# Kernel tuning notes

Hardware: AMD Instinct MI355X
Metric: run time of the kernel (lower is better)

The kernel has to match this reference:

```python
import jax, jax.numpy as jnp
import numpy as np

P_F, P_E = 64, 64
S_F, S_E = 64, 64
W_F, W_E = 32, 32
FH, FO = 256, 128
PR_F, PR_E = 32, 32
VI_F, VI_E = 32, 32
RE_F, RE_E = 32, 32
H1, H2 = 64, 32
GH, NHEADS = 32, 4
DH = PR_E + VI_E + RE_E + P_E + S_E  # 224, hypernetwork input dim
FUSE_IN = 2 * P_E + 2 * S_E + W_E    # 288
N_COLL = 200000
M_NODES = 2048


def setup_inputs() -> dict:
    key = jax.random.key(0)
    ks = jax.random.split(key, 40)
    rn = lambda k, s, sc=1.0: jax.random.normal(k, s, jnp.float32) * sc
    W = 0.05
    inp = {
        'x_u_profile': rn(ks[0], (1, P_F)),
        'x_u_shopping': rn(ks[1], (1, S_F)),
        'x_u_workplace': rn(ks[2], (1, W_F)),
        'x_u_colleague_p': rn(ks[3], (N_COLL, P_F)),
        'x_u_colleague_s': rn(ks[4], (N_COLL, S_F)),
        'x_h_property': rn(ks[5], (1, PR_F)),
        'x_h_vicinity': rn(ks[6], (1, VI_F)),
        'x_h_reachability': rn(ks[7], (1, RE_F)),
        'x_h_neighborhood_p': rn(ks[8], (M_NODES, P_F)),
        'x_h_neighborhood_s': rn(ks[9], (M_NODES, S_F)),
        'x_h_neighborhood_g': jax.random.randint(ks[10], (M_NODES, M_NODES), 0, 2, jnp.int32),
        'W_up': rn(ks[11], (P_F, P_E), W), 'b_up': jnp.zeros((P_E,), jnp.float32),
        'W_us': rn(ks[12], (S_F, S_E), W), 'b_us': jnp.zeros((S_E,), jnp.float32),
        'W_uw': rn(ks[13], (W_F, W_E), W), 'b_uw': jnp.zeros((W_E,), jnp.float32),
        'v_w': rn(ks[14], (2 * (P_E + S_E), 1), W),
        'W_f1': rn(ks[15], (FUSE_IN, FH), W), 'b_f1': jnp.zeros((FH,), jnp.float32),
        'W_f2': rn(ks[16], (FH, FO), W), 'b_f2': jnp.zeros((FO,), jnp.float32),
        'W_m1': rn(ks[17], (FO, DH * H1), W), 'b_m1': jnp.zeros((DH * H1,), jnp.float32),
        'W_m2': rn(ks[18], (FO, H1 * H2), W), 'b_m2': jnp.zeros((H1 * H2,), jnp.float32),
        'W_m3': rn(ks[19], (FO, H2), W), 'b_m3': jnp.zeros((H2,), jnp.float32),
        'W_hp': rn(ks[20], (PR_F, PR_E), W), 'b_hp': jnp.zeros((PR_E,), jnp.float32),
        'W_hv': rn(ks[21], (VI_F, VI_E), W), 'b_hv': jnp.zeros((VI_E,), jnp.float32),
        'W_hr': rn(ks[22], (RE_F, RE_E), W), 'b_hr': jnp.zeros((RE_E,), jnp.float32),
        'Wg': rn(ks[23], (NHEADS, P_E + S_E, GH), W),
        'ag': rn(ks[24], (NHEADS, 2 * GH, 1), W),
        'Wo': rn(ks[25], (NHEADS * GH, P_E + S_E), W),
        'ao': rn(ks[26], (2 * (P_E + S_E), 1), W),
    }
    return inp


def _forward(x_u_profile, x_u_shopping, x_u_workplace, x_u_colleague_p, x_u_colleague_s,
             x_h_property, x_h_vicinity, x_h_reachability,
             x_h_neighborhood_p, x_h_neighborhood_s,
             W_up, b_up, W_us, b_us, W_uw, b_uw, v_w,
             W_f1, b_f1, W_f2, b_f2,
             W_m1, b_m1, W_m2, b_m2, W_m3, b_m3,
             W_hp, b_hp, W_hv, b_hv, W_hr, b_hr,
             Wg, ag, Wo, ao, adj):
    celu, relu = jax.nn.celu, jax.nn.relu
    # user embeddings (batch = 1)
    u_p = celu(x_u_profile @ W_up + b_up)    # [1, P_E]
    u_s = celu(x_u_shopping @ W_us + b_us)   # [1, S_E]
    u_w = celu(x_u_workplace @ W_uw + b_uw)  # [1, W_E]
    # colleague embeddings (shared embedding weights)
    c_p = celu(x_u_colleague_p @ W_up + b_up)  # [N, P_E]
    c_s = celu(x_u_colleague_s @ W_us + b_us)  # [N, S_E]
    n = c_p.shape[0]
    # expand user (shopping, profile) to colleague set and attend
    exp = jnp.concatenate([jnp.broadcast_to(u_s, (n, S_E)),
                           jnp.broadcast_to(u_p, (n, P_E))], axis=1)
    concat = jnp.concatenate([exp, c_p, c_s], axis=1)        # [N, 2*(P_E+S_E)]
    atten = jax.nn.softmax(concat @ v_w, axis=0)             # [N, 1]
    coll = jnp.concatenate([c_p, c_s], axis=1)               # [N, P_E+S_E]
    x_coll = (atten.T @ coll) / n                            # [1, P_E+S_E]
    # user fusion
    fu = jnp.concatenate([u_p, u_s, u_w, x_coll], axis=1)    # [1, FUSE_IN]
    x_u = celu(celu(fu @ W_f1 + b_f1) @ W_f2 + b_f2)         # [1, FO]
    # hypernetwork-generated weights
    w1 = celu(x_u @ W_m1 + b_m1).reshape(DH, H1)
    w2 = celu(x_u @ W_m2 + b_m2).reshape(H1, H2)
    w3 = celu(x_u @ W_m3 + b_m3).reshape(H2, 1)
    # house embeddings
    h_p = celu(x_h_property @ W_hp + b_hp)
    h_v = celu(x_h_vicinity @ W_hv + b_hv)
    h_r = celu(x_h_reachability @ W_hr + b_hr)
    # neighborhood GAT over dense adjacency
    n_p = celu(x_h_neighborhood_p @ W_up + b_up)
    n_s = celu(x_h_neighborhood_s @ W_us + b_us)
    gx = jnp.concatenate([n_p, n_s], axis=1)                 # [M, P_E+S_E]
    mask = adj > 0

    def gat_layer(x, Wl, al):
        h = x @ Wl                                            # [M, F]
        f = h.shape[1]
        f1 = h @ al[:f]                                       # [M, 1]
        f2 = h @ al[f:]                                       # [M, 1]
        e = jax.nn.leaky_relu(f1 + f2.T, 0.2)                 # [M, M]
        e = jnp.where(mask, e, -1e9)
        att = jax.nn.softmax(e, axis=1)
        return att @ h

    heads = jax.vmap(lambda Wl, al: jax.nn.elu(gat_layer(gx, Wl, al)))(Wg, ag)  # [H, M, GH]
    hcat = jnp.transpose(heads, (1, 0, 2)).reshape(gx.shape[0], NHEADS * GH)
    gat_out = jax.nn.elu(gat_layer(hcat, Wo, ao))             # [M, P_E+S_E]
    neigh = gat_out.mean(axis=0, keepdims=True)               # [1, P_E+S_E]
    x_h = jnp.concatenate([h_p, h_v, h_r, neigh], axis=1)     # [1, DH]
    # meta_fcn: per-user generated MLP applied to house features
    return jax.nn.sigmoid(relu(relu(x_h @ w1) @ w2) @ w3)     # [1, 1]


def reference(x_u_profile, x_u_shopping, x_u_workplace, x_u_colleague_p, x_u_colleague_s,
              x_h_property, x_h_vicinity, x_h_reachability,
              x_h_neighborhood_p, x_h_neighborhood_s, x_h_neighborhood_g,
              W_up, b_up, W_us, b_us, W_uw, b_uw, v_w,
              W_f1, b_f1, W_f2, b_f2,
              W_m1, b_m1, W_m2, b_m2, W_m3, b_m3,
              W_hp, b_hp, W_hv, b_hv, W_hr, b_hr,
              Wg, ag, Wo, ao):
    return _forward(x_u_profile, x_u_shopping, x_u_workplace, x_u_colleague_p, x_u_colleague_s,
                    x_h_property, x_h_vicinity, x_h_reachability,
                    x_h_neighborhood_p, x_h_neighborhood_s,
                    W_up, b_up, W_us, b_us, W_uw, b_uw, v_w,
                    W_f1, b_f1, W_f2, b_f2,
                    W_m1, b_m1, W_m2, b_m2, W_m3, b_m3,
                    W_hp, b_hp, W_hv, b_hv, W_hr, b_hr,
                    Wg, ag, Wo, ao, x_h_neighborhood_g)
```

## Files before the change

kernel.cpp:

```cpp
#include <hip/hip_runtime.h>
#include <math.h>

#define N_COLL 200000

typedef const float* fp;
typedef __attribute__((ext_vector_type(8))) short bf16x8;
typedef __attribute__((ext_vector_type(4))) float f32x4;

#define WS_UP    0
#define WS_US    64
#define WS_UW    128
#define WS_HP    160
#define WS_HV    192
#define WS_HR    224
#define WS_XU    384
#define WS_W1    512
#define WS_W2    14848
#define WS_W3    16896
#define WS_NEIGH 16928
#define WS_CSUM  18976
#define WS_GX    23552
#define WS_HT1   285696
#define WS_F1G   416768
#define WS_F2G   424960
#define WS_HCAT  433152
#define WS_HT2   695296
#define WS_F1O   826368
#define WS_F2O   828416
#define WS_MASK  830464

__device__ __forceinline__ float celu1(float x){
    return fmaxf(x, 0.f) + __expf(fminf(x, 0.f)) - 1.f;
}
__device__ __forceinline__ float rl(float x, int k){
    return __int_as_float(__builtin_amdgcn_readlane(__float_as_int(x), k));
}
__device__ __forceinline__ short f2bf(float f){
    return (short)(__float_as_uint(f) >> 16);
}
__device__ __forceinline__ bf16x8 pack8(f32x4 a, f32x4 b){
    bf16x8 r;
    r[0]=f2bf(a[0]); r[1]=f2bf(a[1]); r[2]=f2bf(a[2]); r[3]=f2bf(a[3]);
    r[4]=f2bf(b[0]); r[5]=f2bf(b[1]); r[6]=f2bf(b[2]); r[7]=f2bf(b[3]);
    return r;
}

__global__ __launch_bounds__(256) void kA(
    fp Xcp, fp Xcs, fp vw,
    fp xup, fp xus, fp xuw, fp xhp, fp xhv, fp xhr,
    fp Wup, fp bup, fp Wus, fp bus, fp Wuw, fp buw,
    fp Whp, fp bhp, fp Whv, fp bhv, fp Whr, fp bhr,
    fp Xnp, fp Xns, const int* __restrict__ adj, float* ws)
{
    __shared__ float smem[8720];
    int t = threadIdx.x;
    int b = blockIdx.x;
    if (b < 768){
        float* sW = smem;
        float* sRed = smem + 8192;
        for (int i = t; i < 4096; i += 256){ sW[i] = Wup[i]; sW[4096+i] = Wus[i]; }
        __syncthreads();
        const int lane = t & 63, wv = t >> 6;
        const int q = lane >> 4, c16 = lane & 15;

        bf16x8 B[2][2][4];
        float bias[8], vv[8];
        #pragma unroll
        for (int mat = 0; mat < 2; ++mat)
          #pragma unroll
          for (int ks = 0; ks < 2; ++ks)
            #pragma unroll
            for (int ct = 0; ct < 4; ++ct){
                bf16x8 f;
                #pragma unroll
                for (int j = 0; j < 8; ++j)
                    f[j] = f2bf(sW[mat*4096 + (ks*32 + q*8 + j)*64 + ct*16 + c16]);
                B[mat][ks][ct] = f;
            }
        #pragma unroll
        for (int tt = 0; tt < 8; ++tt){
            int gcol = tt*16 + c16;
            bias[tt] = (tt < 4) ? bup[gcol] : bus[gcol-64];
            vv[tt]   = vw[128 + gcol];
        }

        const int wave = b*4 + wv;
        float accw[8] = {0,0,0,0,0,0,0,0};
        float accl = 0.f;

        int rt = wave;
        f32x4 L[8];
        {
            int row = rt*16 + c16;
            const float* xp = Xcp + row*64 + q*8;
            const float* xs = Xcs + row*64 + q*8;
            L[0]=*(const f32x4*)(xp);    L[1]=*(const f32x4*)(xp+4);
            L[2]=*(const f32x4*)(xp+32); L[3]=*(const f32x4*)(xp+36);
            L[4]=*(const f32x4*)(xs);    L[5]=*(const f32x4*)(xs+4);
            L[6]=*(const f32x4*)(xs+32); L[7]=*(const f32x4*)(xs+36);
        }
        while (rt < 12500){
            int nrt = rt + 3072;
            f32x4 N[8];
            if (nrt < 12500){
                int row = nrt*16 + c16;
                const float* xp = Xcp + row*64 + q*8;
                const float* xs = Xcs + row*64 + q*8;
                N[0]=*(const f32x4*)(xp);    N[1]=*(const f32x4*)(xp+4);
                N[2]=*(const f32x4*)(xp+32); N[3]=*(const f32x4*)(xp+36);
                N[4]=*(const f32x4*)(xs);    N[5]=*(const f32x4*)(xs+4);
                N[6]=*(const f32x4*)(xs+32); N[7]=*(const f32x4*)(xs+36);
            }
            bf16x8 Ap0 = pack8(L[0],L[1]);
            bf16x8 Ap1 = pack8(L[2],L[3]);
            bf16x8 As0 = pack8(L[4],L[5]);
            bf16x8 As1 = pack8(L[6],L[7]);

            float cel[8][4];
            float logit[4] = {0,0,0,0};
            #pragma unroll
            for (int tt = 0; tt < 8; ++tt){
                int ct = tt & 3;
                f32x4 c = {0.f,0.f,0.f,0.f};
                if (tt < 4){
                    c = __builtin_amdgcn_mfma_f32_16x16x32_bf16(Ap0, B[0][0][ct], c, 0,0,0);
                    c = __builtin_amdgcn_mfma_f32_16x16x32_bf16(Ap1, B[0][1][ct], c, 0,0,0);
                } else {
                    c = __builtin_amdgcn_mfma_f32_16x16x32_bf16(As0, B[1][0][ct], c, 0,0,0);
                    c = __builtin_amdgcn_mfma_f32_16x16x32_bf16(As1, B[1][1][ct], c, 0,0,0);
                }
                #pragma unroll
                for (int r = 0; r < 4; ++r){
                    float v = celu1(c[r] + bias[tt]);
                    cel[tt][r] = v;
                    logit[r] = fmaf(v, vv[tt], logit[r]);
                }
            }
            #pragma unroll
            for (int d = 1; d < 16; d <<= 1){
                #pragma unroll
                for (int r = 0; r < 4; ++r) logit[r] += __shfl_xor(logit[r], d);
            }
            float p[4];
            #pragma unroll
            for (int r = 0; r < 4; ++r){ p[r] = __expf(logit[r]); accl += p[r]; }
            #pragma unroll
            for (int tt = 0; tt < 8; ++tt)
                #pragma unroll
                for (int r = 0; r < 4; ++r) accw[tt] = fmaf(p[r], cel[tt][r], accw[tt]);
            #pragma unroll
            for (int i = 0; i < 8; ++i) L[i] = N[i];
            rt = nrt;
        }
        #pragma unroll
        for (int tt = 0; tt < 8; ++tt){
            accw[tt] += __shfl_xor(accw[tt], 16);
            accw[tt] += __shfl_xor(accw[tt], 32);
        }
        accl += __shfl_xor(accl, 16);
        accl += __shfl_xor(accl, 32);
        if (q == 0){
            #pragma unroll
            for (int tt = 0; tt < 8; ++tt) sRed[wv*132 + tt*16 + c16] = accw[tt];
        }
        if (lane == 0) sRed[wv*132 + 128] = accl;
        __syncthreads();
        if (t < 129){
            float s = sRed[t] + sRed[132+t] + sRed[264+t] + sRed[396+t];
            atomicAdd(ws + WS_CSUM + (b & 31)*132 + t, s);
        }
    } else if (b < 1280){
        unsigned* mb = (unsigned*)(ws + WS_MASK);
        int idx = (b-768)*256 + t;
        const int* a = adj + (idx>>6)*2048 + (idx&63)*32;
        unsigned bits = 0u;
        #pragma unroll 8
        for (int j = 0; j < 32; ++j) bits |= (a[j] > 0 ? 1u : 0u) << j;
        mb[idx] = bits;
    } else if (b < 1408){
        float* sWp = smem;
        float* sWs = smem + 4096;
        float* sbp = smem + 8192;
        float* sbs = smem + 8256;
        int b2 = b - 1280;
        for (int i = t; i < 4096; i += 256){ sWp[i] = Wup[i]; sWs[i] = Wus[i]; }
        if (t < 64){ sbp[t]=bup[t]; sbs[t]=bus[t]; }
        __syncthreads();
        int lane = t & 63, wave = (b2<<2) | (t>>6);
        for (int r = wave; r < 2048; r += 512){
            float xp = Xnp[(r<<6)+lane], xs = Xns[(r<<6)+lane];
            float cp = sbp[lane], cs = sbs[lane];
            #pragma unroll 8
            for (int k = 0; k < 64; ++k){
                cp = fmaf(rl(xp,k), sWp[(k<<6)+lane], cp);
                cs = fmaf(rl(xs,k), sWs[(k<<6)+lane], cs);
            }
            ws[WS_GX + (r<<7) + lane]      = celu1(cp);
            ws[WS_GX + (r<<7) + 64 + lane] = celu1(cs);
        }
    } else {
        if (t < 64){
            float acc = bup[t];
            for (int k = 0; k < 64; ++k) acc = fmaf(xup[k], Wup[k*64+t], acc);
            ws[WS_UP+t] = celu1(acc);
        } else if (t < 128){
            int j = t-64; float acc = bus[j];
            for (int k = 0; k < 64; ++k) acc = fmaf(xus[k], Wus[k*64+j], acc);
            ws[WS_US+j] = celu1(acc);
        } else if (t < 160){
            int j = t-128; float acc = buw[j];
            for (int k = 0; k < 32; ++k) acc = fmaf(xuw[k], Wuw[k*32+j], acc);
            ws[WS_UW+j] = celu1(acc);
        } else if (t < 192){
            int j = t-160; float acc = bhp[j];
            for (int k = 0; k < 32; ++k) acc = fmaf(xhp[k], Whp[k*32+j], acc);
            ws[WS_HP+j] = celu1(acc);
        } else if (t < 224){
            int j = t-192; float acc = bhv[j];
            for (int k = 0; k < 32; ++k) acc = fmaf(xhv[k], Whv[k*32+j], acc);
            ws[WS_HV+j] = celu1(acc);
        } else {
            int j = t-224; float acc = bhr[j];
            for (int k = 0; k < 32; ++k) acc = fmaf(xhr[k], Whr[k*32+j], acc);
            ws[WS_HR+j] = celu1(acc);
        }
    }
}

__global__ __launch_bounds__(256) void kB(fp Wg, fp ag, fp Wf1, fp bf1, fp Wf2, fp bf2, float* ws){
    __shared__ float smem[673];
    int t = threadIdx.x;
    int b = blockIdx.x;
    if (b < 128){
        int lane = t & 63;
        int wave = (b<<2) | (t>>6);
        int h1 = lane>>5, h2 = 2 + (lane>>5), g = lane & 31;
        float agh1a = ag[h1*64+g], agh1b = ag[h1*64+32+g];
        float agh2a = ag[h2*64+g], agh2b = ag[h2*64+32+g];
        unsigned short* ht = (unsigned short*)(ws + WS_HT1);
        for (int r = wave; r < 2048; r += 512){
            const float* gx = ws + WS_GX + (r<<7);
            float x1 = gx[lane], x2 = gx[64+lane];
            float a1 = 0.f, a2 = 0.f;
            #pragma unroll 4
            for (int k = 0; k < 64; ++k){
                float gk = rl(x1,k);
                a1 = fmaf(gk, Wg[h1*4096 + (k<<5) + g], a1);
                a2 = fmaf(gk, Wg[h2*4096 + (k<<5) + g], a2);
            }
            #pragma unroll 4
            for (int k = 0; k < 64; ++k){
                float gk = rl(x2,k);
                a1 = fmaf(gk, Wg[h1*4096 + ((64+k)<<5) + g], a1);
                a2 = fmaf(gk, Wg[h2*4096 + ((64+k)<<5) + g], a2);
            }
            ht[lane*2048 + r]      = (unsigned short)f2bf(a1);
            ht[(64+lane)*2048 + r] = (unsigned short)f2bf(a2);
            float s1 = a1*agh1a, t1 = a1*agh1b, s2 = a2*agh2a, t2 = a2*agh2b;
            #pragma unroll
            for (int d = 1; d < 32; d <<= 1){
                s1 += __shfl_xor(s1,d); t1 += __shfl_xor(t1,d);
                s2 += __shfl_xor(s2,d); t2 += __shfl_xor(t2,d);
            }
            if ((lane&31) == 0){
                int hh = lane>>5;
                ws[WS_F1G + (hh<<11) + r] = s1;
                ws[WS_F2G + (hh<<11) + r] = t1;
                ws[WS_F1G + ((hh+2)<<11) + r] = s2;
                ws[WS_F2G + ((hh+2)<<11) + r] = t2;
            }
        }
    } else {
        float* fu  = smem;
        float* hid = smem + 288;
        float* cs  = smem + 544;
        if (t < 129){
            float s = 0.f;
            #pragma unroll
            for (int k = 0; k < 32; ++k) s += ws[WS_CSUM + k*132 + t];
            cs[t] = s;
        }
        if (t < 64)       fu[t] = ws[WS_UP + t];
        else if (t < 128) fu[t] = ws[WS_US + t-64];
        else if (t < 160) fu[t] = ws[WS_UW + t-128];
        __syncthreads();
        if (t < 128) fu[160 + t] = cs[t] / (cs[128] * (float)N_COLL);
        __syncthreads();
        float acc = bf1[t];
        for (int k = 0; k < 288; ++k) acc = fmaf(fu[k], Wf1[k*256+t], acc);
        hid[t] = celu1(acc);
        __syncthreads();
        if (t < 128){
            float a2 = bf2[t];
            for (int k = 0; k < 256; ++k) a2 = fmaf(hid[k], Wf2[k*128+t], a2);
            ws[WS_XU + t] = celu1(a2);
        }
    }
}

__global__ __launch_bounds__(256) void kC(fp Wm1, fp bm1, fp Wm2, fp bm2, fp Wm3, fp bm3, float* ws){
    __shared__ float smem[2112];
    int t = threadIdx.x;
    int b = blockIdx.x;
    if (b < 512){
        float* Cs = smem;
        float* Sp = smem + 2048;
        int w = t >> 6, lane = t & 63;
        int q = lane >> 4, c16 = lane & 15;
        int rt = b >> 2, h = b & 3;
        int row = rt*16 + c16;
        const unsigned* mb = (const unsigned*)(ws + WS_MASK) + row*64;
        const unsigned short* HT = (const unsigned short*)(ws + WS_HT1) + h*32*2048;
        float f1 = ws[WS_F1G + (h<<11) + row];
        const float* f2 = ws + WS_F2G + (h<<11);
        f32x4 c0 = {0,0,0,0}, c1 = {0,0,0,0};
        float S = 0.f;
        for (int kt = w*16; kt < w*16 + 16; ++kt){
            unsigned m32 = mb[kt];
            const float* f2p = f2 + kt*32 + q*8;
            f32x4 fa = *(const f32x4*)(f2p);
            f32x4 fb = *(const f32x4*)(f2p+4);
            bf16x8 A;
            #pragma unroll
            for (int j = 0; j < 8; ++j){
                float e = f1 + ((j<4) ? fa[j] : fb[j-4]);
                e = fmaxf(e, 0.2f*e);
                float p = ((m32 >> (q*8+j)) & 1u) ? __expf(e) : 0.f;
                unsigned short pb = (unsigned short)(__float_as_uint(p) >> 16);
                A[j] = (short)pb;
                S += __uint_as_float(((unsigned)pb) << 16);
            }
            bf16x8 B0 = *(const bf16x8*)(HT + (c16)*2048    + kt*32 + q*8);
            bf16x8 B1 = *(const bf16x8*)(HT + (16+c16)*2048 + kt*32 + q*8);
            c0 = __builtin_amdgcn_mfma_f32_16x16x32_bf16(A, B0, c0, 0,0,0);
            c1 = __builtin_amdgcn_mfma_f32_16x16x32_bf16(A, B1, c1, 0,0,0);
        }
        S += __shfl_xor(S, 16);
        S += __shfl_xor(S, 32);
        if (q == 0) Sp[w*16 + c16] = S;
        #pragma unroll
        for (int r = 0; r < 4; ++r){
            Cs[w*512 + (q*4+r)*32 + c16]      = c0[r];
            Cs[w*512 + (q*4+r)*32 + 16 + c16] = c1[r];
        }
        __syncthreads();
        for (int ee = t; ee < 512; ee += 256){
            int r = ee >> 5, cc = ee & 31;
            float v = Cs[r*32+cc] + Cs[512 + r*32+cc] + Cs[1024 + r*32+cc] + Cs[1536 + r*32+cc];
            float Ss = Sp[r] + Sp[16+r] + Sp[32+r] + Sp[48+r];
            ws[WS_HCAT + (rt*16 + r)*128 + h*32 + cc] = celu1(v / Ss);
        }
    } else {
        float* xu = smem;
        if (t < 128) xu[t] = ws[WS_XU + t];
        __syncthreads();
        int j = (b - 512)*256 + t;
        if (j < 14336){
            float acc = bm1[j];
            for (int k = 0; k < 128; ++k) acc = fmaf(xu[k], Wm1[k*14336 + j], acc);
            ws[WS_W1 + j] = celu1(acc);
        } else if (j < 16384){
            int j2 = j - 14336;
            float acc = bm2[j2];
            for (int k = 0; k < 128; ++k) acc = fmaf(xu[k], Wm2[k*2048 + j2], acc);
            ws[WS_W2 + j2] = celu1(acc);
        } else if (j < 16416){
            int j3 = j - 16384;
            float acc = bm3[j3];
            for (int k = 0; k < 128; ++k) acc = fmaf(xu[k], Wm3[k*32 + j3], acc);
            ws[WS_W3 + j3] = celu1(acc);
        }
    }
}

__global__ __launch_bounds__(256) void l2_proj(fp Wo, fp ao, float* ws){
    int t = threadIdx.x, lane = t & 63;
    int wave = (blockIdx.x<<2) | (t>>6);
    float aoa1 = ao[lane],     aoa2 = ao[64+lane];
    float aob1 = ao[128+lane], aob2 = ao[192+lane];
    unsigned short* ht = (unsigned short*)(ws + WS_HT2);
    for (int r = wave; r < 2048; r += 512){
        const float* hc = ws + WS_HCAT + (r<<7);
        float x1 = hc[lane], x2 = hc[64+lane];
        float a1 = 0.f, a2 = 0.f;
        #pragma unroll 4
        for (int k = 0; k < 64; ++k){
            float gk = rl(x1,k);
            a1 = fmaf(gk, Wo[(k<<7)+lane], a1);
            a2 = fmaf(gk, Wo[(k<<7)+64+lane], a2);
        }
        #pragma unroll 4
        for (int k = 0; k < 64; ++k){
            float gk = rl(x2,k);
            a1 = fmaf(gk, Wo[((64+k)<<7)+lane], a1);
            a2 = fmaf(gk, Wo[((64+k)<<7)+64+lane], a2);
        }
        ht[lane*2048 + r]      = (unsigned short)f2bf(a1);
        ht[(64+lane)*2048 + r] = (unsigned short)f2bf(a2);
        float s = a1*aoa1 + a2*aoa2;
        float u = a1*aob1 + a2*aob2;
        #pragma unroll
        for (int d = 1; d < 64; d <<= 1){ s += __shfl_xor(s,d); u += __shfl_xor(u,d); }
        if (lane == 0){ ws[WS_F1O + r] = s; ws[WS_F2O + r] = u; }
    }
}

__global__ __launch_bounds__(256) void attend2(float* ws){
    __shared__ float Cs[4][16][128];
    __shared__ float Sp[4][16];
    __shared__ float colp[2][128];
    int t = threadIdx.x;
    int w = t >> 6, lane = t & 63;
    int q = lane >> 4, c16 = lane & 15;
    int rt = blockIdx.x;
    int row = rt*16 + c16;
    const unsigned* mb = (const unsigned*)(ws + WS_MASK) + row*64;
    const unsigned short* HT = (const unsigned short*)(ws + WS_HT2);
    float f1 = ws[WS_F1O + row];
    const float* f2 = ws + WS_F2O;
    f32x4 c[8];
    #pragma unroll
    for (int nt = 0; nt < 8; ++nt) c[nt] = (f32x4){0,0,0,0};
    float S = 0.f;
    for (int kt = w*16; kt < w*16 + 16; ++kt){
        unsigned m32 = mb[kt];
        const float* f2p = f2 + kt*32 + q*8;
        f32x4 fa = *(const f32x4*)(f2p);
        f32x4 fb = *(const f32x4*)(f2p+4);
        bf16x8 A;
        #pragma unroll
        for (int j = 0; j < 8; ++j){
            float e = f1 + ((j<4) ? fa[j] : fb[j-4]);
            e = fmaxf(e, 0.2f*e);
            float p = ((m32 >> (q*8+j)) & 1u) ? __expf(e) : 0.f;
            unsigned short pb = (unsigned short)(__float_as_uint(p) >> 16);
            A[j] = (short)pb;
            S += __uint_as_float(((unsigned)pb) << 16);
        }
        #pragma unroll
        for (int nt = 0; nt < 8; ++nt){
            bf16x8 B = *(const bf16x8*)(HT + (nt*16 + c16)*2048 + kt*32 + q*8);
            c[nt] = __builtin_amdgcn_mfma_f32_16x16x32_bf16(A, B, c[nt], 0,0,0);
        }
    }
    S += __shfl_xor(S, 16);
    S += __shfl_xor(S, 32);
    if (q == 0) Sp[w][c16] = S;
    #pragma unroll
    for (int nt = 0; nt < 8; ++nt)
        #pragma unroll
        for (int r = 0; r < 4; ++r)
            Cs[w][q*4+r][nt*16+c16] = c[nt][r];
    __syncthreads();
    int col = t & 127, half = t >> 7;
    float part = 0.f;
    for (int r = half*8; r < half*8 + 8; ++r){
        float v = Cs[0][r][col] + Cs[1][r][col] + Cs[2][r][col] + Cs[3][r][col];
        float Ss = Sp[0][r] + Sp[1][r] + Sp[2][r] + Sp[3][r];
        part += celu1(v / Ss);
    }
    colp[half][col] = part;
    __syncthreads();
    if (t < 128) atomicAdd(ws + WS_NEIGH + (blockIdx.x & 15)*128 + t, colp[0][t] + colp[1][t]);
}

__global__ __launch_bounds__(256) void final_k(float* ws, float* out){
    __shared__ float xh[224], r1[64], r2[32];
    int t = threadIdx.x;
    if (t < 32)       xh[t]      = ws[WS_HP + t];
    else if (t < 64)  xh[t]      = ws[WS_HV + t-32];
    else if (t < 96)  xh[t]      = ws[WS_HR + t-64];
    if (t < 128){
        float s = 0.f;
        #pragma unroll
        for (int k = 0; k < 16; ++k) s += ws[WS_NEIGH + k*128 + t];
        xh[96 + t] = s * (1.f/2048.f);
    }
    __syncthreads();
    if (t < 64){
        float acc = 0.f;
        for (int k = 0; k < 224; ++k) acc = fmaf(xh[k], ws[WS_W1 + k*64 + t], acc);
        r1[t] = fmaxf(acc, 0.f);
    }
    __syncthreads();
    if (t < 32){
        float acc = 0.f;
        for (int k = 0; k < 64; ++k) acc = fmaf(r1[k], ws[WS_W2 + k*32 + t], acc);
        r2[t] = fmaxf(acc, 0.f);
    }
    __syncthreads();
    if (t == 0){
        float acc = 0.f;
        for (int k = 0; k < 32; ++k) acc = fmaf(r2[k], ws[WS_W3 + k], acc);
        out[0] = 1.f / (1.f + __expf(-acc));
    }
}

extern "C" void kernel_launch(void* const* d_in, const int* in_sizes, int n_in,
                              void* d_out, int out_size, void* d_ws, size_t ws_size,
                              hipStream_t stream)
{
    fp xup = (fp)d_in[0],  xus = (fp)d_in[1],  xuw = (fp)d_in[2];
    fp Xcp = (fp)d_in[3],  Xcs = (fp)d_in[4];
    fp xhp = (fp)d_in[5],  xhv = (fp)d_in[6],  xhr = (fp)d_in[7];
    fp Xnp = (fp)d_in[8],  Xns = (fp)d_in[9];
    const int* adj = (const int*)d_in[10];
    fp Wup = (fp)d_in[11], bup = (fp)d_in[12];
    fp Wus = (fp)d_in[13], bus = (fp)d_in[14];
    fp Wuw = (fp)d_in[15], buw = (fp)d_in[16];
    fp vw  = (fp)d_in[17];
    fp Wf1 = (fp)d_in[18], bf1 = (fp)d_in[19];
    fp Wf2 = (fp)d_in[20], bf2 = (fp)d_in[21];
    fp Wm1 = (fp)d_in[22], bm1 = (fp)d_in[23];
    fp Wm2 = (fp)d_in[24], bm2 = (fp)d_in[25];
    fp Wm3 = (fp)d_in[26], bm3 = (fp)d_in[27];
    fp Whp = (fp)d_in[28], bhp = (fp)d_in[29];
    fp Whv = (fp)d_in[30], bhv = (fp)d_in[31];
    fp Whr = (fp)d_in[32], bhr = (fp)d_in[33];
    fp Wg  = (fp)d_in[34], ag  = (fp)d_in[35];
    fp Wo  = (fp)d_in[36], ao  = (fp)d_in[37];
    float* ws = (float*)d_ws;
    float* out = (float*)d_out;

    hipMemsetAsync((char*)d_ws + WS_NEIGH*sizeof(float), 0, 6272*sizeof(float), stream);

    kA<<<1409, 256, 0, stream>>>(Xcp,Xcs,vw, xup,xus,xuw,xhp,xhv,xhr,
                                 Wup,bup,Wus,bus,Wuw,buw,Whp,bhp,Whv,bhv,Whr,bhr,
                                 Xnp,Xns, adj, ws);
    kB<<<129, 256, 0, stream>>>(Wg, ag, Wf1,bf1,Wf2,bf2, ws);
    kC<<<577, 256, 0, stream>>>(Wm1,bm1,Wm2,bm2,Wm3,bm3, ws);
    l2_proj<<<128, 256, 0, stream>>>(Wo, ao, ws);
    attend2<<<128, 256, 0, stream>>>(ws);
    final_k<<<1, 256, 0, stream>>>(ws, out);
}
```

Before: 349.2 us.

## Fuse all stages into one persistent kernel with grid-wide barriers

Merges the six kernel launches into one 512-block persistent kernel that separates stages with software grid barriers built on atomic counters in workspace. The Wg and Wo projections are redone with bf16 MFMA tiles in place of scalar readlane FMA loops, the adjacency-mask and small-projection work is redistributed over fewer blocks, and the colleague-encoder loop now covers more rows per wave. This removes launch gaps and speeds the projections, at the cost of a spin barrier that deadlocks unless all 512 blocks are co-resident, and less parallelism in the colleague scan.

```diff
diff --git a/kernel.cpp b/kernel.cpp
--- a/kernel.cpp
+++ b/kernel.cpp
@@ -6,6 +6,7 @@
 typedef const float* fp;
 typedef __attribute__((ext_vector_type(8))) short bf16x8;
 typedef __attribute__((ext_vector_type(4))) float f32x4;
+typedef __attribute__((ext_vector_type(4))) short s16x4;
 
 #define WS_UP    0
 #define WS_US    64
@@ -19,6 +20,7 @@
 #define WS_W3    16896
 #define WS_NEIGH 16928
 #define WS_CSUM  18976
+#define WS_BAR   23200
 #define WS_GX    23552
 #define WS_HT1   285696
 #define WS_F1G   416768
@@ -45,49 +47,62 @@
     return r;
 }
 
-__global__ __launch_bounds__(256) void kA(
-    fp Xcp, fp Xcs, fp vw,
-    fp xup, fp xus, fp xuw, fp xhp, fp xhv, fp xhr,
-    fp Wup, fp bup, fp Wus, fp bus, fp Wuw, fp buw,
+#define GRID_N 512u
+__device__ __forceinline__ void gbar(float* ws, int which){
+    unsigned* c = (unsigned*)(ws + WS_BAR) + which;
+    __syncthreads();
+    if (threadIdx.x == 0){
+        __threadfence();
+        atomicAdd(c, 1u);
+        while (atomicAdd(c, 0u) < GRID_N) __builtin_amdgcn_s_sleep(8);
+        __threadfence();
+    }
+    __syncthreads();
+}
+
+__global__ __launch_bounds__(256, 2) void mega(
+    fp xup, fp xus, fp xuw, fp Xcp, fp Xcs,
+    fp xhp, fp xhv, fp xhr, fp Xnp, fp Xns, const int* __restrict__ adj,
+    fp Wup, fp bup, fp Wus, fp bus, fp Wuw, fp buw, fp vw,
+    fp Wf1, fp bf1, fp Wf2, fp bf2,
+    fp Wm1, fp bm1, fp Wm2, fp bm2, fp Wm3, fp bm3,
     fp Whp, fp bhp, fp Whv, fp bhv, fp Whr, fp bhr,
-    fp Xnp, fp Xns, const int* __restrict__ adj, float* ws)
+    fp Wg, fp ag, fp Wo, fp ao,
+    float* ws, float* out)
 {
-    __shared__ float smem[8720];
-    int t = threadIdx.x;
-    int b = blockIdx.x;
-    if (b < 768){
-        float* sW = smem;
-        float* sRed = smem + 8192;
-        for (int i = t; i < 4096; i += 256){ sW[i] = Wup[i]; sW[4096+i] = Wus[i]; }
-        __syncthreads();
-        const int lane = t & 63, wv = t >> 6;
-        const int q = lane >> 4, c16 = lane & 15;
-
+    __shared__ float smem[8512];
+    const int t = threadIdx.x;
+    const int b = blockIdx.x;
+    const int lane = t & 63, wv = t >> 6;
+    const int q = lane >> 4, c16 = lane & 15;
+
+    if (b < 384){
+        float* sRed = smem;
         bf16x8 B[2][2][4];
         float bias[8], vv[8];
         #pragma unroll
-        for (int mat = 0; mat < 2; ++mat)
-          #pragma unroll
-          for (int ks = 0; ks < 2; ++ks)
-            #pragma unroll
-            for (int ct = 0; ct < 4; ++ct){
-                bf16x8 f;
+        for (int mat = 0; mat < 2; ++mat){
+            fp W = mat ? Wus : Wup;
+            #pragma unroll
+            for (int ks = 0; ks < 2; ++ks)
                 #pragma unroll
-                for (int j = 0; j < 8; ++j)
-                    f[j] = f2bf(sW[mat*4096 + (ks*32 + q*8 + j)*64 + ct*16 + c16]);
-                B[mat][ks][ct] = f;
-            }
+                for (int ct = 0; ct < 4; ++ct){
+                    bf16x8 f;
+                    #pragma unroll
+                    for (int j = 0; j < 8; ++j)
+                        f[j] = f2bf(W[(ks*32 + q*8 + j)*64 + ct*16 + c16]);
+                    B[mat][ks][ct] = f;
+                }
+        }
         #pragma unroll
         for (int tt = 0; tt < 8; ++tt){
             int gcol = tt*16 + c16;
             bias[tt] = (tt < 4) ? bup[gcol] : bus[gcol-64];
             vv[tt]   = vw[128 + gcol];
         }
-
         const int wave = b*4 + wv;
         float accw[8] = {0,0,0,0,0,0,0,0};
         float accl = 0.f;
-
         int rt = wave;
         f32x4 L[8];
         {
@@ -100,7 +115,7 @@
             L[6]=*(const f32x4*)(xs+32); L[7]=*(const f32x4*)(xs+36);
         }
         while (rt < 12500){
-            int nrt = rt + 3072;
+            int nrt = rt + 1536;
             f32x4 N[8];
             if (nrt < 12500){
                 int row = nrt*16 + c16;
@@ -115,7 +130,6 @@
             bf16x8 Ap1 = pack8(L[2],L[3]);
             bf16x8 As0 = pack8(L[4],L[5]);
             bf16x8 As1 = pack8(L[6],L[7]);
-
             float cel[8][4];
             float logit[4] = {0,0,0,0};
             #pragma unroll
@@ -169,25 +183,54 @@
             float s = sRed[t] + sRed[132+t] + sRed[264+t] + sRed[396+t];
             atomicAdd(ws + WS_CSUM + (b & 31)*132 + t, s);
         }
-    } else if (b < 1280){
+    } else if (b < 448){
         unsigned* mb = (unsigned*)(ws + WS_MASK);
-        int idx = (b-768)*256 + t;
-        const int* a = adj + (idx>>6)*2048 + (idx&63)*32;
-        unsigned bits = 0u;
-        #pragma unroll 8
-        for (int j = 0; j < 32; ++j) bits |= (a[j] > 0 ? 1u : 0u) << j;
-        mb[idx] = bits;
-    } else if (b < 1408){
+        #pragma unroll
+        for (int s = 0; s < 8; ++s){
+            int idx = (b-384)*2048 + s*256 + t;
+            const int* a = adj + (idx>>6)*2048 + (idx&63)*32;
+            unsigned bits = 0u;
+            #pragma unroll 8
+            for (int j = 0; j < 32; ++j) bits |= (a[j] > 0 ? 1u : 0u) << j;
+            mb[idx] = bits;
+        }
+        if (b == 384){
+            if (t < 64){
+                float acc = bup[t];
+                for (int k = 0; k < 64; ++k) acc = fmaf(xup[k], Wup[k*64+t], acc);
+                ws[WS_UP+t] = celu1(acc);
+            } else if (t < 128){
+                int j = t-64; float acc = bus[j];
+                for (int k = 0; k < 64; ++k) acc = fmaf(xus[k], Wus[k*64+j], acc);
+                ws[WS_US+j] = celu1(acc);
+            } else if (t < 160){
+                int j = t-128; float acc = buw[j];
+                for (int k = 0; k < 32; ++k) acc = fmaf(xuw[k], Wuw[k*32+j], acc);
+                ws[WS_UW+j] = celu1(acc);
+            } else if (t < 192){
+                int j = t-160; float acc = bhp[j];
+                for (int k = 0; k < 32; ++k) acc = fmaf(xhp[k], Whp[k*32+j], acc);
+                ws[WS_HP+j] = celu1(acc);
+            } else if (t < 224){
+                int j = t-192; float acc = bhv[j];
+                for (int k = 0; k < 32; ++k) acc = fmaf(xhv[k], Whv[k*32+j], acc);
+                ws[WS_HV+j] = celu1(acc);
+            } else {
+                int j = t-224; float acc = bhr[j];
+                for (int k = 0; k < 32; ++k) acc = fmaf(xhr[k], Whr[k*32+j], acc);
+                ws[WS_HR+j] = celu1(acc);
+            }
+        }
+    } else {
         float* sWp = smem;
         float* sWs = smem + 4096;
         float* sbp = smem + 8192;
         float* sbs = smem + 8256;
-        int b2 = b - 1280;
         for (int i = t; i < 4096; i += 256){ sWp[i] = Wup[i]; sWs[i] = Wus[i]; }
         if (t < 64){ sbp[t]=bup[t]; sbs[t]=bus[t]; }
         __syncthreads();
-        int lane = t & 63, wave = (b2<<2) | (t>>6);
-        for (int r = wave; r < 2048; r += 512){
+        int wave = ((b-448)<<2) | wv;
+        for (int r = wave; r < 2048; r += 256){
             float xp = Xnp[(r<<6)+lane], xs = Xns[(r<<6)+lane];
             float cp = sbp[lane], cs = sbs[lane];
             #pragma unroll 8
@@ -198,79 +241,58 @@
             ws[WS_GX + (r<<7) + lane]      = celu1(cp);
             ws[WS_GX + (r<<7) + 64 + lane] = celu1(cs);
         }
-    } else {
-        if (t < 64){
-            float acc = bup[t];
-            for (int k = 0; k < 64; ++k) acc = fmaf(xup[k], Wup[k*64+t], acc);
-            ws[WS_UP+t] = celu1(acc);
-        } else if (t < 128){
-            int j = t-64; float acc = bus[j];
-            for (int k = 0; k < 64; ++k) acc = fmaf(xus[k], Wus[k*64+j], acc);
-            ws[WS_US+j] = celu1(acc);
-        } else if (t < 160){
-            int j = t-128; float acc = buw[j];
-            for (int k = 0; k < 32; ++k) acc = fmaf(xuw[k], Wuw[k*32+j], acc);
-            ws[WS_UW+j] = celu1(acc);
-        } else if (t < 192){
-            int j = t-160; float acc = bhp[j];
-            for (int k = 0; k < 32; ++k) acc = fmaf(xhp[k], Whp[k*32+j], acc);
-            ws[WS_HP+j] = celu1(acc);
-        } else if (t < 224){
-            int j = t-192; float acc = bhv[j];
-            for (int k = 0; k < 32; ++k) acc = fmaf(xhv[k], Whv[k*32+j], acc);
-            ws[WS_HV+j] = celu1(acc);
-        } else {
-            int j = t-224; float acc = bhr[j];
-            for (int k = 0; k < 32; ++k) acc = fmaf(xhr[k], Whr[k*32+j], acc);
-            ws[WS_HR+j] = celu1(acc);
-        }
-    }
-}
-
-__global__ __launch_bounds__(256) void kB(fp Wg, fp ag, fp Wf1, fp bf1, fp Wf2, fp bf2, float* ws){
-    __shared__ float smem[673];
-    int t = threadIdx.x;
-    int b = blockIdx.x;
+    }
+    gbar(ws, 0);
+
     if (b < 128){
-        int lane = t & 63;
-        int wave = (b<<2) | (t>>6);
-        int h1 = lane>>5, h2 = 2 + (lane>>5), g = lane & 31;
-        float agh1a = ag[h1*64+g], agh1b = ag[h1*64+32+g];
-        float agh2a = ag[h2*64+g], agh2b = ag[h2*64+32+g];
+        int rt = b, w = wv;
+        bf16x8 A[4];
+        const float* gxr = ws + WS_GX + (rt*16 + c16)*128;
+        #pragma unroll
+        for (int kt = 0; kt < 4; ++kt)
+            A[kt] = pack8(*(const f32x4*)(gxr + kt*32 + q*8),
+                          *(const f32x4*)(gxr + kt*32 + q*8 + 4));
         unsigned short* ht = (unsigned short*)(ws + WS_HT1);
-        for (int r = wave; r < 2048; r += 512){
-            const float* gx = ws + WS_GX + (r<<7);
-            float x1 = gx[lane], x2 = gx[64+lane];
-            float a1 = 0.f, a2 = 0.f;
-            #pragma unroll 4
-            for (int k = 0; k < 64; ++k){
-                float gk = rl(x1,k);
-                a1 = fmaf(gk, Wg[h1*4096 + (k<<5) + g], a1);
-                a2 = fmaf(gk, Wg[h2*4096 + (k<<5) + g], a2);
-            }
-            #pragma unroll 4
-            for (int k = 0; k < 64; ++k){
-                float gk = rl(x2,k);
-                a1 = fmaf(gk, Wg[h1*4096 + ((64+k)<<5) + g], a1);
-                a2 = fmaf(gk, Wg[h2*4096 + ((64+k)<<5) + g], a2);
-            }
-            ht[lane*2048 + r]      = (unsigned short)f2bf(a1);
-            ht[(64+lane)*2048 + r] = (unsigned short)f2bf(a2);
-            float s1 = a1*agh1a, t1 = a1*agh1b, s2 = a2*agh2a, t2 = a2*agh2b;
-            #pragma unroll
-            for (int d = 1; d < 32; d <<= 1){
-                s1 += __shfl_xor(s1,d); t1 += __shfl_xor(t1,d);
-                s2 += __shfl_xor(s2,d); t2 += __shfl_xor(t2,d);
-            }
-            if ((lane&31) == 0){
-                int hh = lane>>5;
-                ws[WS_F1G + (hh<<11) + r] = s1;
-                ws[WS_F2G + (hh<<11) + r] = t1;
-                ws[WS_F1G + ((hh+2)<<11) + r] = s2;
-                ws[WS_F2G + ((hh+2)<<11) + r] = t2;
-            }
-        }
-    } else {
+        float f1p[4] = {0,0,0,0}, f2p[4] = {0,0,0,0};
+        #pragma unroll
+        for (int ct = 0; ct < 2; ++ct){
+            int g = ct*16 + c16;
+            f32x4 c = {0,0,0,0};
+            #pragma unroll
+            for (int kt = 0; kt < 4; ++kt){
+                bf16x8 Bf;
+                #pragma unroll
+                for (int j = 0; j < 8; ++j)
+                    Bf[j] = f2bf(Wg[w*4096 + (kt*32 + q*8 + j)*32 + g]);
+                c = __builtin_amdgcn_mfma_f32_16x16x32_bf16(A[kt], Bf, c, 0,0,0);
+            }
+            int col = w*32 + g;
+            s16x4 pk;
+            pk[0]=f2bf(c[0]); pk[1]=f2bf(c[1]); pk[2]=f2bf(c[2]); pk[3]=f2bf(c[3]);
+            *(s16x4*)(ht + col*2048 + rt*16 + q*4) = pk;
+            float aga = ag[w*64 + g], agb = ag[w*64 + 32 + g];
+            #pragma unroll
+            for (int r = 0; r < 4; ++r){
+                f1p[r] = fmaf(c[r], aga, f1p[r]);
+                f2p[r] = fmaf(c[r], agb, f2p[r]);
+            }
+        }
+        #pragma unroll
+        for (int d = 1; d < 16; d <<= 1){
+            #pragma unroll
+            for (int r = 0; r < 4; ++r){
+                f1p[r] += __shfl_xor(f1p[r], d);
+                f2p[r] += __shfl_xor(f2p[r], d);
+            }
+        }
+        if (c16 == 0){
+            #pragma unroll
+            for (int r = 0; r < 4; ++r){
+                ws[WS_F1G + (w<<11) + rt*16 + q*4 + r] = f1p[r];
+                ws[WS_F2G + (w<<11) + rt*16 + q*4 + r] = f2p[r];
+            }
+        }
+    } else if (b == 128){
         float* fu  = smem;
         float* hid = smem + 288;
         float* cs  = smem + 544;
@@ -296,17 +318,12 @@
             ws[WS_XU + t] = celu1(a2);
         }
     }
-}
-
-__global__ __launch_bounds__(256) void kC(fp Wm1, fp bm1, fp Wm2, fp bm2, fp Wm3, fp bm3, float* ws){
-    __shared__ float smem[2112];
-    int t = threadIdx.x;
-    int b = blockIdx.x;
-    if (b < 512){
+    gbar(ws, 1);
+
+    {
         float* Cs = smem;
         float* Sp = smem + 2048;
-        int w = t >> 6, lane = t & 63;
-        int q = lane >> 4, c16 = lane & 15;
+        int w = wv;
         int rt = b >> 2, h = b & 3;
         int row = rt*16 + c16;
         const unsigned* mb = (const unsigned*)(ws + WS_MASK) + row*64;
@@ -350,11 +367,68 @@
             float Ss = Sp[r] + Sp[16+r] + Sp[32+r] + Sp[48+r];
             ws[WS_HCAT + (rt*16 + r)*128 + h*32 + cc] = celu1(v / Ss);
         }
-    } else {
+    }
+    gbar(ws, 2);
+
+    if (b < 128){
+        int rt = b, w = wv;
+        bf16x8 A[4];
+        const float* hcr = ws + WS_HCAT + (rt*16 + c16)*128;
+        #pragma unroll
+        for (int kt = 0; kt < 4; ++kt)
+            A[kt] = pack8(*(const f32x4*)(hcr + kt*32 + q*8),
+                          *(const f32x4*)(hcr + kt*32 + q*8 + 4));
+        unsigned short* ht = (unsigned short*)(ws + WS_HT2);
+        float f1p[4] = {0,0,0,0}, f2p[4] = {0,0,0,0};
+        #pragma unroll
+        for (int ct = 0; ct < 2; ++ct){
+            int col = w*32 + ct*16 + c16;
+            f32x4 c = {0,0,0,0};
+            #pragma unroll
+            for (int kt = 0; kt < 4; ++kt){
+                bf16x8 Bf;
+                #pragma unroll
+                for (int j = 0; j < 8; ++j)
+                    Bf[j] = f2bf(Wo[(kt*32 + q*8 + j)*128 + col]);
+                c = __builtin_amdgcn_mfma_f32_16x16x32_bf16(A[kt], Bf, c, 0,0,0);
+            }
+            s16x4 pk;
+            pk[0]=f2bf(c[0]); pk[1]=f2bf(c[1]); pk[2]=f2bf(c[2]); pk[3]=f2bf(c[3]);
+            *(s16x4*)(ht + col*2048 + rt*16 + q*4) = pk;
+            float aoa = ao[col], aob = ao[128 + col];
+            #pragma unroll
+            for (int r = 0; r < 4; ++r){
+                f1p[r] = fmaf(c[r], aoa, f1p[r]);
+                f2p[r] = fmaf(c[r], aob, f2p[r]);
+            }
+        }
+        #pragma unroll
+        for (int d = 1; d < 16; d <<= 1){
+            #pragma unroll
+            for (int r = 0; r < 4; ++r){
+                f1p[r] += __shfl_xor(f1p[r], d);
+                f2p[r] += __shfl_xor(f2p[r], d);
+            }
+        }
+        if (c16 == 0){
+            #pragma unroll
+            for (int r = 0; r < 4; ++r){
+                smem[w*16 + q*4 + r]      = f1p[r];
+                smem[64 + w*16 + q*4 + r] = f2p[r];
+            }
+        }
+        __syncthreads();
+        if (t < 16){
+            float s = smem[t] + smem[16+t] + smem[32+t] + smem[48+t];
+            float u = smem[64+t] + smem[80+t] + smem[96+t] + smem[112+t];
+            ws[WS_F1O + rt*16 + t] = s;
+            ws[WS_F2O + rt*16 + t] = u;
+        }
+    } else if (b < 193){
         float* xu = smem;
         if (t < 128) xu[t] = ws[WS_XU + t];
         __syncthreads();
-        int j = (b - 512)*256 + t;
+        int j = (b - 128)*256 + t;
         if (j < 14336){
             float acc = bm1[j];
             for (int k = 0; k < 128; ++k) acc = fmaf(xu[k], Wm1[k*14336 + j], acc);
@@ -371,128 +445,97 @@
             ws[WS_W3 + j3] = celu1(acc);
         }
     }
-}
-
-__global__ __launch_bounds__(256) void l2_proj(fp Wo, fp ao, float* ws){
-    int t = threadIdx.x, lane = t & 63;
-    int wave = (blockIdx.x<<2) | (t>>6);
-    float aoa1 = ao[lane],     aoa2 = ao[64+lane];
-    float aob1 = ao[128+lane], aob2 = ao[192+lane];
-    unsigned short* ht = (unsigned short*)(ws + WS_HT2);
-    for (int r = wave; r < 2048; r += 512){
-        const float* hc = ws + WS_HCAT + (r<<7);
-        float x1 = hc[lane], x2 = hc[64+lane];
-        float a1 = 0.f, a2 = 0.f;
-        #pragma unroll 4
-        for (int k = 0; k < 64; ++k){
-            float gk = rl(x1,k);
-            a1 = fmaf(gk, Wo[(k<<7)+lane], a1);
-            a2 = fmaf(gk, Wo[(k<<7)+64+lane], a2);
-        }
-        #pragma unroll 4
-        for (int k = 0; k < 64; ++k){
-            float gk = rl(x2,k);
-            a1 = fmaf(gk, Wo[((64+k)<<7)+lane], a1);
-            a2 = fmaf(gk, Wo[((64+k)<<7)+64+lane], a2);
-        }
-        ht[lane*2048 + r]      = (unsigned short)f2bf(a1);
-        ht[(64+lane)*2048 + r] = (unsigned short)f2bf(a2);
-        float s = a1*aoa1 + a2*aoa2;
-        float u = a1*aob1 + a2*aob2;
-        #pragma unroll
-        for (int d = 1; d < 64; d <<= 1){ s += __shfl_xor(s,d); u += __shfl_xor(u,d); }
-        if (lane == 0){ ws[WS_F1O + r] = s; ws[WS_F2O + r] = u; }
-    }
-}
-
-__global__ __launch_bounds__(256) void attend2(float* ws){
-    __shared__ float Cs[4][16][128];
-    __shared__ float Sp[4][16];
-    __shared__ float colp[2][128];
-    int t = threadIdx.x;
-    int w = t >> 6, lane = t & 63;
-    int q = lane >> 4, c16 = lane & 15;
-    int rt = blockIdx.x;
-    int row = rt*16 + c16;
-    const unsigned* mb = (const unsigned*)(ws + WS_MASK) + row*64;
-    const unsigned short* HT = (const unsigned short*)(ws + WS_HT2);
-    float f1 = ws[WS_F1O + row];
-    const float* f2 = ws + WS_F2O;
-    f32x4 c[8];
-    #pragma unroll
-    for (int nt = 0; nt < 8; ++nt) c[nt] = (f32x4){0,0,0,0};
-    float S = 0.f;
-    for (int kt = w*16; kt < w*16 + 16; ++kt){
-        unsigned m32 = mb[kt];
-        const float* f2p = f2 + kt*32 + q*8;
-        f32x4 fa = *(const f32x4*)(f2p);
-        f32x4 fb = *(const f32x4*)(f2p+4);
-        bf16x8 A;
-        #pragma unroll
-        for (int j = 0; j < 8; ++j){
-            float e = f1 + ((j<4) ? fa[j] : fb[j-4]);
-            e = fmaxf(e, 0.2f*e);
-            float p = ((m32 >> (q*8+j)) & 1u) ? __expf(e) : 0.f;
-            unsigned short pb = (unsigned short)(__float_as_uint(p) >> 16);
-            A[j] = (short)pb;
-            S += __uint_as_float(((unsigned)pb) << 16);
-        }
-        #pragma unroll
-        for (int nt = 0; nt < 8; ++nt){
-            bf16x8 B = *(const bf16x8*)(HT + (nt*16 + c16)*2048 + kt*32 + q*8);
-            c[nt] = __builtin_amdgcn_mfma_f32_16x16x32_bf16(A, B, c[nt], 0,0,0);
-        }
-    }
-    S += __shfl_xor(S, 16);
-    S += __shfl_xor(S, 32);
-    if (q == 0) Sp[w][c16] = S;
-    #pragma unroll
-    for (int nt = 0; nt < 8; ++nt)
-        #pragma unroll
-        for (int r = 0; r < 4; ++r)
-            Cs[w][q*4+r][nt*16+c16] = c[nt][r];
-    __syncthreads();
-    int col = t & 127, half = t >> 7;
-    float part = 0.f;
-    for (int r = half*8; r < half*8 + 8; ++r){
-        float v = Cs[0][r][col] + Cs[1][r][col] + Cs[2][r][col] + Cs[3][r][col];
-        float Ss = Sp[0][r] + Sp[1][r] + Sp[2][r] + Sp[3][r];
-        part += celu1(v / Ss);
-    }
-    colp[half][col] = part;
-    __syncthreads();
-    if (t < 128) atomicAdd(ws + WS_NEIGH + (blockIdx.x & 15)*128 + t, colp[0][t] + colp[1][t]);
-}
-
-__global__ __launch_bounds__(256) void final_k(float* ws, float* out){
-    __shared__ float xh[224], r1[64], r2[32];
-    int t = threadIdx.x;
-    if (t < 32)       xh[t]      = ws[WS_HP + t];
-    else if (t < 64)  xh[t]      = ws[WS_HV + t-32];
-    else if (t < 96)  xh[t]      = ws[WS_HR + t-64];
-    if (t < 128){
-        float s = 0.f;
-        #pragma unroll
-        for (int k = 0; k < 16; ++k) s += ws[WS_NEIGH + k*128 + t];
-        xh[96 + t] = s * (1.f/2048.f);
-    }
-    __syncthreads();
-    if (t < 64){
-        float acc = 0.f;
-        for (int k = 0; k < 224; ++k) acc = fmaf(xh[k], ws[WS_W1 + k*64 + t], acc);
-        r1[t] = fmaxf(acc, 0.f);
-    }
-    __syncthreads();
-    if (t < 32){
-        float acc = 0.f;
-        for (int k = 0; k < 64; ++k) acc = fmaf(r1[k], ws[WS_W2 + k*32 + t], acc);
-        r2[t] = fmaxf(acc, 0.f);
-    }
-    __syncthreads();
-    if (t == 0){
-        float acc = 0.f;
-        for (int k = 0; k < 32; ++k) acc = fmaf(r2[k], ws[WS_W3 + k], acc);
-        out[0] = 1.f / (1.f + __expf(-acc));
+    gbar(ws, 3);
+
+    if (b < 128){
+        float* Cs   = smem;
+        float* Sp   = smem + 8192;
+        float* colp = smem + 8256;
+        int w = wv;
+        int rt = b;
+        int row = rt*16 + c16;
+        const unsigned* mb = (const unsigned*)(ws + WS_MASK) + row*64;
+        const unsigned short* HT = (const unsigned short*)(ws + WS_HT2);
+        float f1 = ws[WS_F1O + row];
+        const float* f2 = ws + WS_F2O;
+        f32x4 c[8];
+        #pragma unroll
+        for (int nt = 0; nt < 8; ++nt) c[nt] = (f32x4){0,0,0,0};
+        float S = 0.f;
+        for (int kt = w*16; kt < w*16 + 16; ++kt){
+            unsigned m32 = mb[kt];
+            const float* f2p = f2 + kt*32 + q*8;
+            f32x4 fa = *(const f32x4*)(f2p);
+            f32x4 fb = *(const f32x4*)(f2p+4);
+            bf16x8 A;
+            #pragma unroll
+            for (int j = 0; j < 8; ++j){
+                float e = f1 + ((j<4) ? fa[j] : fb[j-4]);
+                e = fmaxf(e, 0.2f*e);
+                float p = ((m32 >> (q*8+j)) & 1u) ? __expf(e) : 0.f;
+                unsigned short pb = (unsigned short)(__float_as_uint(p) >> 16);
+                A[j] = (short)pb;
+                S += __uint_as_float(((unsigned)pb) << 16);
+            }
+            #pragma unroll
+            for (int nt = 0; nt < 8; ++nt){
+                bf16x8 B = *(const bf16x8*)(HT + (nt*16 + c16)*2048 + kt*32 + q*8);
+                c[nt] = __builtin_amdgcn_mfma_f32_16x16x32_bf16(A, B, c[nt], 0,0,0);
+            }
+        }
+        S += __shfl_xor(S, 16);
+        S += __shfl_xor(S, 32);
+        if (q == 0) Sp[w*16 + c16] = S;
+        #pragma unroll
+        for (int nt = 0; nt < 8; ++nt)
+            #pragma unroll
+            for (int r = 0; r < 4; ++r)
+                Cs[w*2048 + (q*4+r)*128 + nt*16 + c16] = c[nt][r];
+        __syncthreads();
+        int col = t & 127, half = t >> 7;
+        float part = 0.f;
+        for (int r = half*8; r < half*8 + 8; ++r){
+            float v = Cs[r*128+col] + Cs[2048 + r*128+col] + Cs[4096 + r*128+col] + Cs[6144 + r*128+col];
+            float Ss = Sp[r] + Sp[16+r] + Sp[32+r] + Sp[48+r];
+            part += celu1(v / Ss);
+        }
+        colp[half*128 + col] = part;
+        __syncthreads();
+        if (t < 128) atomicAdd(ws + WS_NEIGH + (b & 15)*128 + t, colp[t] + colp[128+t]);
+    }
+    gbar(ws, 4);
+
+    if (b == 0){
+        float* xh = smem;
+        float* r1 = smem + 224;
+        float* r2 = smem + 288;
+        if (t < 32)       xh[t]      = ws[WS_HP + t];
+        else if (t < 64)  xh[t]      = ws[WS_HV + t-32];
+        else if (t < 96)  xh[t]      = ws[WS_HR + t-64];
+        if (t < 128){
+            float s = 0.f;
+            #pragma unroll
+            for (int k = 0; k < 16; ++k) s += ws[WS_NEIGH + k*128 + t];
+            xh[96 + t] = s * (1.f/2048.f);
+        }
+        __syncthreads();
+        if (t < 64){
+            float acc = 0.f;
+            for (int k = 0; k < 224; ++k) acc = fmaf(xh[k], ws[WS_W1 + k*64 + t], acc);
+            r1[t] = fmaxf(acc, 0.f);
+        }
+        __syncthreads();
+        if (t < 32){
+            float acc = 0.f;
+            for (int k = 0; k < 64; ++k) acc = fmaf(r1[k], ws[WS_W2 + k*32 + t], acc);
+            r2[t] = fmaxf(acc, 0.f);
+        }
+        __syncthreads();
+        if (t == 0){
+            float acc = 0.f;
+            for (int k = 0; k < 32; ++k) acc = fmaf(r2[k], ws[WS_W3 + k], acc);
+            out[0] = 1.f / (1.f + __expf(-acc));
+        }
     }
 }
 
@@ -522,14 +565,11 @@
     float* ws = (float*)d_ws;
     float* out = (float*)d_out;
 
-    hipMemsetAsync((char*)d_ws + WS_NEIGH*sizeof(float), 0, 6272*sizeof(float), stream);
-
-    kA<<<1409, 256, 0, stream>>>(Xcp,Xcs,vw, xup,xus,xuw,xhp,xhv,xhr,
-                                 Wup,bup,Wus,bus,Wuw,buw,Whp,bhp,Whv,bhv,Whr,bhr,
-                                 Xnp,Xns, adj, ws);
-    kB<<<129, 256, 0, stream>>>(Wg, ag, Wf1,bf1,Wf2,bf2, ws);
-    kC<<<577, 256, 0, stream>>>(Wm1,bm1,Wm2,bm2,Wm3,bm3, ws);
-    l2_proj<<<128, 256, 0, stream>>>(Wo, ao, ws);
-    attend2<<<128, 256, 0, stream>>>(ws);
-    final_k<<<1, 256, 0, stream>>>(ws, out);
-}
+    hipMemsetAsync((char*)d_ws + WS_NEIGH*sizeof(float), 0, 6280*sizeof(float), stream);
+
+    mega<<<GRID_N, 256, 0, stream>>>(
+        xup,xus,xuw,Xcp,Xcs, xhp,xhv,xhr,Xnp,Xns, adj,
+        Wup,bup,Wus,bus,Wuw,buw,vw,
+        Wf1,bf1,Wf2,bf2, Wm1,bm1,Wm2,bm2,Wm3,bm3,
+        Whp,bhp,Whv,bhv,Whr,bhr, Wg,ag,Wo,ao, ws, out);
+}
```

Result: slower. 498.4 us (+42.7%).
